# Performance work log

Measured on AMD Instinct MI355X. Metric: run time of the kernel, lower is better.

The kernel has to match this reference:

```python
import jax, jax.numpy as jnp
import numpy as np

EMBED_DIM = 2048
HIDDEN_DIM = 2048
SEQ_LEN = 8192


def setup_inputs() -> dict:
    key = jax.random.key(0)
    ks = jax.random.split(key, 6)
    x = jax.random.normal(ks[0], (SEQ_LEN, EMBED_DIM), dtype=jnp.float32)
    # original uses torch.rand (uniform [0,1)) for params
    W_h = jax.random.uniform(ks[1], (HIDDEN_DIM, HIDDEN_DIM), dtype=jnp.float32)
    W_x = jax.random.uniform(ks[2], (HIDDEN_DIM, EMBED_DIM), dtype=jnp.float32)
    W_y = jax.random.uniform(ks[3], (EMBED_DIM, HIDDEN_DIM), dtype=jnp.float32)
    B_h = jax.random.uniform(ks[4], (HIDDEN_DIM,), dtype=jnp.float32)
    B_y = jax.random.uniform(ks[5], (EMBED_DIM,), dtype=jnp.float32)
    return {"x": x, "W_h": W_h, "W_x": W_x, "W_y": W_y, "B_h": B_h, "B_y": B_y}


def reference(x, W_h, W_x, W_y, B_h, B_y):
    # Precompute input projections for all timesteps in one GEMM: [T, H]
    xp = x @ W_x.T + B_h

    def step(h, xp_t):
        h_new = jnp.tanh(W_h @ h + xp_t)  # [H]
        return h_new, h_new

    h0 = jnp.zeros((W_h.shape[0],), dtype=x.dtype)
    h_final, hs = jax.lax.scan(step, h0, xp)  # hs: [T, H]
    # Output projection + softmax over embed dim, batched over timesteps
    logits = hs @ W_y.T + B_y  # [T, E]
    output = jax.nn.softmax(logits, axis=-1)
    return (h_final, output)
```

## Files before the change

kernel.cpp:

```cpp
#include <hip/hip_runtime.h>

#define T_SEQ 8192
#define HDIM  2048
#define EDIM  2048
#define RBLK  64
#define ROWS_PER_BLK (HDIM / RBLK)

typedef unsigned long long u64;
typedef __attribute__((ext_vector_type(4))) unsigned int u32x4;
typedef __attribute__((ext_vector_type(4))) float f32x4;

__device__ inline void poll_pair(const u64* p0, const u64* p1, u32x4& a, u32x4& b) {
    asm volatile("global_load_dwordx4 %0, %2, off sc1\n\t"
                 "global_load_dwordx4 %1, %3, off sc1\n\t"
                 "s_waitcnt vmcnt(0)"
                 : "=v"(a), "=v"(b) : "v"(p0), "v"(p1) : "memory");
}

__device__ inline f32x4 ld_w16(const float* p) {
    f32x4 r;
    asm volatile("global_load_dwordx4 %0, %1, off" : "=v"(r) : "v"(p));
    return r;
}

__device__ inline float fast_tanh(float z) {
    float zc = fminf(fmaxf(z, -15.f), 15.f);
    float zs = zc * 2.88539008177792681f;
    float ez; asm("v_exp_f32 %0, %1" : "=v"(ez) : "v"(zs));
    float rc; float ezp = ez + 1.f;
    asm("v_rcp_f32 %0, %1" : "=v"(rc) : "v"(ezp));
    return (ez - 1.f) * rc;
}

__global__ __launch_bounds__(256) void gemm_nt_bias(
    const float* __restrict__ A, const float* __restrict__ B,
    const float* __restrict__ bias, float* __restrict__ C,
    int M, int N, int K)
{
    constexpr int BK = 32;
    __shared__ float As[BK][64 + 4];
    __shared__ float Bs[BK][64 + 4];

    const int tx = threadIdx.x & 15;
    const int ty = threadIdx.x >> 4;
    const int m0 = blockIdx.y * 64;
    const int n0 = blockIdx.x * 64;

    float acc[4][4] = {};

    for (int kk = 0; kk < K; kk += BK) {
        #pragma unroll
        for (int p = 0; p < 8; ++p) {
            int idx = p * 256 + threadIdx.x;
            int r = idx >> 5;
            int c = idx & 31;
            As[c][r] = A[(size_t)(m0 + r) * K + kk + c];
            Bs[c][r] = B[(size_t)(n0 + r) * K + kk + c];
        }
        __syncthreads();
        #pragma unroll
        for (int k = 0; k < BK; ++k) {
            float4 a = *(const float4*)&As[k][ty * 4];
            float4 b = *(const float4*)&Bs[k][tx * 4];
            float av[4] = {a.x, a.y, a.z, a.w};
            float bv[4] = {b.x, b.y, b.z, b.w};
            #pragma unroll
            for (int i = 0; i < 4; ++i)
                #pragma unroll
                for (int j = 0; j < 4; ++j)
                    acc[i][j] = fmaf(av[i], bv[j], acc[i][j]);
        }
        __syncthreads();
    }

    float4 bb = *(const float4*)&bias[n0 + tx * 4];
    float bvv[4] = {bb.x, bb.y, bb.z, bb.w};
    #pragma unroll
    for (int i = 0; i < 4; ++i) {
        float4 o;
        o.x = acc[i][0] + bvv[0];
        o.y = acc[i][1] + bvv[1];
        o.z = acc[i][2] + bvv[2];
        o.w = acc[i][3] + bvv[3];
        *(float4*)&C[(size_t)(m0 + ty * 4 + i) * N + n0 + tx * 4] = o;
    }
}

__global__ __launch_bounds__(256) void gemm_nt_bias_tc(
    const float* __restrict__ A, const float* __restrict__ B,
    const float* __restrict__ bias, float* __restrict__ Ct,
    int M, int N, int K)
{
    constexpr int BK = 32;
    __shared__ float As[BK][64 + 4];
    __shared__ float Bs[BK][64 + 4];

    const int tx = threadIdx.x & 15;
    const int ty = threadIdx.x >> 4;
    const int m0 = blockIdx.y * 64;
    const int n0 = blockIdx.x * 64;

    float acc[4][4] = {};

    for (int kk = 0; kk < K; kk += BK) {
        #pragma unroll
        for (int p = 0; p < 8; ++p) {
            int idx = p * 256 + threadIdx.x;
            int r = idx >> 5;
            int c = idx & 31;
            As[c][r] = A[(size_t)(m0 + r) * K + kk + c];
            Bs[c][r] = B[(size_t)(n0 + r) * K + kk + c];
        }
        __syncthreads();
        #pragma unroll
        for (int k = 0; k < BK; ++k) {
            float4 a = *(const float4*)&As[k][ty * 4];
            float4 b = *(const float4*)&Bs[k][tx * 4];
            float av[4] = {a.x, a.y, a.z, a.w};
            float bv[4] = {b.x, b.y, b.z, b.w};
            #pragma unroll
            for (int i = 0; i < 4; ++i)
                #pragma unroll
                for (int j = 0; j < 4; ++j)
                    acc[i][j] = fmaf(av[i], bv[j], acc[i][j]);
        }
        __syncthreads();
    }

    float4 bb = *(const float4*)&bias[n0 + tx * 4];
    float bvv[4] = {bb.x, bb.y, bb.z, bb.w};
    #pragma unroll
    for (int j = 0; j < 4; ++j) {
        float4 o;
        o.x = acc[0][j] + bvv[j];
        o.y = acc[1][j] + bvv[j];
        o.z = acc[2][j] + bvv[j];
        o.w = acc[3][j] + bvv[j];
        *(float4*)&Ct[(size_t)(n0 + tx * 4 + j) * M + m0 + ty * 4] = o;
    }
}

__global__ __launch_bounds__(512, 1) void rnn_recurrence(
    const float* __restrict__ Wh, const float* __restrict__ xpT,
    float* __restrict__ Hs, u64* __restrict__ hbuf, int T)
{
    const int tid  = threadIdx.x;
    const int lane = tid & 63;
    const int wid  = tid >> 6;
    const int r0   = blockIdx.x * ROWS_PER_BLK + wid * 4;

    const float* wr0 = Wh + (size_t)(r0 + 0) * HDIM + lane * 4;
    const float* wr1 = Wh + (size_t)(r0 + 1) * HDIM + lane * 4;
    const float* wr2 = Wh + (size_t)(r0 + 2) * HDIM + lane * 4;
    const float* wr3 = Wh + (size_t)(r0 + 3) * HDIM + lane * 4;

    f32x4 w00 = ld_w16(wr0 + 0*256), w01 = ld_w16(wr0 + 1*256), w02 = ld_w16(wr0 + 2*256), w03 = ld_w16(wr0 + 3*256);
    f32x4 w04 = ld_w16(wr0 + 4*256), w05 = ld_w16(wr0 + 5*256), w06 = ld_w16(wr0 + 6*256), w07 = ld_w16(wr0 + 7*256);
    f32x4 w10 = ld_w16(wr1 + 0*256), w11 = ld_w16(wr1 + 1*256), w12 = ld_w16(wr1 + 2*256), w13 = ld_w16(wr1 + 3*256);
    f32x4 w14 = ld_w16(wr1 + 4*256), w15 = ld_w16(wr1 + 5*256), w16 = ld_w16(wr1 + 6*256), w17 = ld_w16(wr1 + 7*256);
    f32x4 w20 = ld_w16(wr2 + 0*256), w21 = ld_w16(wr2 + 1*256), w22 = ld_w16(wr2 + 2*256), w23 = ld_w16(wr2 + 3*256);
    f32x4 w24 = ld_w16(wr2 + 4*256), w25 = ld_w16(wr2 + 5*256), w26 = ld_w16(wr2 + 6*256), w27 = ld_w16(wr2 + 7*256);
    f32x4 w30 = ld_w16(wr3 + 0*256), w31 = ld_w16(wr3 + 1*256), w32 = ld_w16(wr3 + 2*256), w33 = ld_w16(wr3 + 3*256);
    f32x4 w34 = ld_w16(wr3 + 4*256), w35 = ld_w16(wr3 + 5*256), w36 = ld_w16(wr3 + 6*256), w37 = ld_w16(wr3 + 7*256);
    asm volatile("s_waitcnt vmcnt(0)" ::: "memory");

    __shared__ float hsm[HDIM];

    for (int t = 0; t < T; ++t) {
        float xq = 0.f;
        if (lane < 4) xq = xpT[(size_t)(r0 + lane) * T + t];

        float sv = 0.f;
        if (t > 0) {
            const u64* hb = hbuf + (size_t)(t & 1) * HDIM;
            const unsigned tg = (unsigned)t;
            const u64* p0 = hb + 2 * tid;
            const u64* p1 = hb + 1024 + 2 * tid;

            u32x4 a, b;
            poll_pair(p0, p1, a, b);
            while ((a.y != tg) | (a.w != tg) | (b.y != tg) | (b.w != tg))
                poll_pair(p0, p1, a, b);

            ((float2*)hsm)[tid] =
                make_float2(__uint_as_float(a.x), __uint_as_float(a.z));
            ((float2*)hsm)[tid + 512] =
                make_float2(__uint_as_float(b.x), __uint_as_float(b.z));
            __syncthreads();

            float s0 = 0.f, s1 = 0.f, s2 = 0.f, s3 = 0.f;
            #define RNN_STEP(IDX, WA, WB, WC, WD)                                   \
            {   float4 h4 = ((const float4*)hsm)[(IDX) * 64 + lane];                \
                s0 = fmaf(WA.x, h4.x, s0); s0 = fmaf(WA.y, h4.y, s0);               \
                s0 = fmaf(WA.z, h4.z, s0); s0 = fmaf(WA.w, h4.w, s0);               \
                s1 = fmaf(WB.x, h4.x, s1); s1 = fmaf(WB.y, h4.y, s1);               \
                s1 = fmaf(WB.z, h4.z, s1); s1 = fmaf(WB.w, h4.w, s1);               \
                s2 = fmaf(WC.x, h4.x, s2); s2 = fmaf(WC.y, h4.y, s2);               \
                s2 = fmaf(WC.z, h4.z, s2); s2 = fmaf(WC.w, h4.w, s2);               \
                s3 = fmaf(WD.x, h4.x, s3); s3 = fmaf(WD.y, h4.y, s3);               \
                s3 = fmaf(WD.z, h4.z, s3); s3 = fmaf(WD.w, h4.w, s3); }
            RNN_STEP(0, w00, w10, w20, w30)
            RNN_STEP(1, w01, w11, w21, w31)
            RNN_STEP(2, w02, w12, w22, w32)
            RNN_STEP(3, w03, w13, w23, w33)
            RNN_STEP(4, w04, w14, w24, w34)
            RNN_STEP(5, w05, w15, w25, w35)
            RNN_STEP(6, w06, w16, w26, w36)
            RNN_STEP(7, w07, w17, w27, w37)
            #undef RNN_STEP

            float fa = (lane & 1) ? s1 : s0;
            float fb = (lane & 1) ? s0 : s1;
            fa += __shfl_xor(fb, 1);
            float fc = (lane & 1) ? s3 : s2;
            float fd = (lane & 1) ? s2 : s3;
            fc += __shfl_xor(fd, 1);
            float fe = (lane & 2) ? fc : fa;
            float ff = (lane & 2) ? fa : fc;
            fe += __shfl_xor(ff, 2);
            #pragma unroll
            for (int off = 4; off < 64; off <<= 1) fe += __shfl_xor(fe, off);
            sv = fe;
        }

        if (lane < 4) {
            float hn = fast_tanh(sv + xq);
            u64 pk = ((u64)(unsigned)(t + 1) << 32) | (u64)__float_as_uint(hn);
            (void)__hip_atomic_exchange(
                &hbuf[(size_t)((t + 1) & 1) * HDIM + r0 + lane], pk,
                __ATOMIC_RELAXED, __HIP_MEMORY_SCOPE_AGENT);
            Hs[(size_t)t * HDIM + r0 + lane] = hn;
        }
    }
}

__global__ __launch_bounds__(256) void softmax_rows(
    const float* __restrict__ logits, float* __restrict__ out)
{
    const int row = blockIdx.x;
    const float4* in4 = (const float4*)(logits + (size_t)row * EDIM);
    float4* out4 = (float4*)(out + (size_t)row * EDIM);

    float4 v0 = in4[threadIdx.x];
    float4 v1 = in4[threadIdx.x + 256];

    float m = fmaxf(fmaxf(fmaxf(v0.x, v0.y), fmaxf(v0.z, v0.w)),
                    fmaxf(fmaxf(v1.x, v1.y), fmaxf(v1.z, v1.w)));
    #pragma unroll
    for (int off = 32; off > 0; off >>= 1) m = fmaxf(m, __shfl_xor(m, off));

    __shared__ float red[4];
    if ((threadIdx.x & 63) == 0) red[threadIdx.x >> 6] = m;
    __syncthreads();
    m = fmaxf(fmaxf(red[0], red[1]), fmaxf(red[2], red[3]));
    __syncthreads();

    float e[8];
    e[0] = expf(v0.x - m); e[1] = expf(v0.y - m);
    e[2] = expf(v0.z - m); e[3] = expf(v0.w - m);
    e[4] = expf(v1.x - m); e[5] = expf(v1.y - m);
    e[6] = expf(v1.z - m); e[7] = expf(v1.w - m);

    float s = e[0] + e[1] + e[2] + e[3] + e[4] + e[5] + e[6] + e[7];
    #pragma unroll
    for (int off = 32; off > 0; off >>= 1) s += __shfl_xor(s, off);
    if ((threadIdx.x & 63) == 0) red[threadIdx.x >> 6] = s;
    __syncthreads();
    s = red[0] + red[1] + red[2] + red[3];

    float inv = 1.0f / s;
    out4[threadIdx.x]       = make_float4(e[0] * inv, e[1] * inv, e[2] * inv, e[3] * inv);
    out4[threadIdx.x + 256] = make_float4(e[4] * inv, e[5] * inv, e[6] * inv, e[7] * inv);
}

__global__ void copy_vec(const float* __restrict__ src, float* __restrict__ dst, int n)
{
    int i = blockIdx.x * blockDim.x + threadIdx.x;
    if (i < n) dst[i] = src[i];
}

extern "C" void kernel_launch(void* const* d_in, const int* in_sizes, int n_in,
                              void* d_out, int out_size, void* d_ws, size_t ws_size,
                              hipStream_t stream)
{
    const float* x  = (const float*)d_in[0];
    const float* Wh = (const float*)d_in[1];
    const float* Wx = (const float*)d_in[2];
    const float* Wy = (const float*)d_in[3];
    const float* Bh = (const float*)d_in[4];
    const float* By = (const float*)d_in[5];

    float* out    = (float*)d_out;
    float* hfinal = out;
    float* hs     = out + HDIM;

    float* xpT  = (float*)d_ws;
    u64*   hbuf = (u64*)((char*)d_ws + (size_t)T_SEQ * HDIM * 4);
    float* logits = xpT;

    hipMemsetAsync(hbuf, 0, 2 * HDIM * sizeof(u64), stream);

    gemm_nt_bias_tc<<<dim3(HDIM / 64, T_SEQ / 64), 256, 0, stream>>>(
        x, Wx, Bh, xpT, T_SEQ, HDIM, EDIM);

    int T = T_SEQ;
    const float* xpT_c = xpT;
    void* args[] = {(void*)&Wh, (void*)&xpT_c, (void*)&hs, (void*)&hbuf, (void*)&T};
    hipLaunchCooperativeKernel((void*)rnn_recurrence, dim3(RBLK), dim3(512),
                               args, 0, stream);

    gemm_nt_bias<<<dim3(EDIM / 64, T_SEQ / 64), 256, 0, stream>>>(
        hs, Wy, By, logits, T_SEQ, EDIM, HDIM);

    copy_vec<<<dim3(HDIM / 256), 256, 0, stream>>>(
        hs + (size_t)(T_SEQ - 1) * HDIM, hfinal, HDIM);

    softmax_rows<<<dim3(T_SEQ), 256, 0, stream>>>(logits, hs);
}
```

Before: 14.82 ms.

## Repartition recurrence so each thread owns a column slice of all block rows

The recurrent matvec is restructured so each thread holds 4 columns for all 32 rows of its block, instead of each wave owning 4 rows across all columns. Each thread now polls only the 4 hidden values it needs from global memory, which drops the shared-memory broadcast of the full hidden state. Partial sums are combined with a multi-row butterfly shuffle, then a shared-memory cross-wave sum performed by a single wave. This trades the full-vector LDS staging for more shuffle work and an extra barrier per step, and concentrates the tanh and publish on one wave.

```diff
diff --git a/kernel.cpp b/kernel.cpp
--- a/kernel.cpp
+++ b/kernel.cpp
@@ -4,7 +4,6 @@
 #define HDIM  2048
 #define EDIM  2048
 #define RBLK  64
-#define ROWS_PER_BLK (HDIM / RBLK)
 
 typedef unsigned long long u64;
 typedef __attribute__((ext_vector_type(4))) unsigned int u32x4;
@@ -147,89 +146,72 @@
     const int tid  = threadIdx.x;
     const int lane = tid & 63;
     const int wid  = tid >> 6;
-    const int r0   = blockIdx.x * ROWS_PER_BLK + wid * 4;
-
-    const float* wr0 = Wh + (size_t)(r0 + 0) * HDIM + lane * 4;
-    const float* wr1 = Wh + (size_t)(r0 + 1) * HDIM + lane * 4;
-    const float* wr2 = Wh + (size_t)(r0 + 2) * HDIM + lane * 4;
-    const float* wr3 = Wh + (size_t)(r0 + 3) * HDIM + lane * 4;
-
-    f32x4 w00 = ld_w16(wr0 + 0*256), w01 = ld_w16(wr0 + 1*256), w02 = ld_w16(wr0 + 2*256), w03 = ld_w16(wr0 + 3*256);
-    f32x4 w04 = ld_w16(wr0 + 4*256), w05 = ld_w16(wr0 + 5*256), w06 = ld_w16(wr0 + 6*256), w07 = ld_w16(wr0 + 7*256);
-    f32x4 w10 = ld_w16(wr1 + 0*256), w11 = ld_w16(wr1 + 1*256), w12 = ld_w16(wr1 + 2*256), w13 = ld_w16(wr1 + 3*256);
-    f32x4 w14 = ld_w16(wr1 + 4*256), w15 = ld_w16(wr1 + 5*256), w16 = ld_w16(wr1 + 6*256), w17 = ld_w16(wr1 + 7*256);
-    f32x4 w20 = ld_w16(wr2 + 0*256), w21 = ld_w16(wr2 + 1*256), w22 = ld_w16(wr2 + 2*256), w23 = ld_w16(wr2 + 3*256);
-    f32x4 w24 = ld_w16(wr2 + 4*256), w25 = ld_w16(wr2 + 5*256), w26 = ld_w16(wr2 + 6*256), w27 = ld_w16(wr2 + 7*256);
-    f32x4 w30 = ld_w16(wr3 + 0*256), w31 = ld_w16(wr3 + 1*256), w32 = ld_w16(wr3 + 2*256), w33 = ld_w16(wr3 + 3*256);
-    f32x4 w34 = ld_w16(wr3 + 4*256), w35 = ld_w16(wr3 + 5*256), w36 = ld_w16(wr3 + 6*256), w37 = ld_w16(wr3 + 7*256);
+    const int r0   = blockIdx.x * 32;
+    const int c0   = tid * 4;
+
+    f32x4 w[32];
+    #pragma unroll
+    for (int r = 0; r < 32; ++r)
+        w[r] = ld_w16(Wh + (size_t)(r0 + r) * HDIM + c0);
     asm volatile("s_waitcnt vmcnt(0)" ::: "memory");
 
-    __shared__ float hsm[HDIM];
+    __shared__ float pw[8 * 32];
 
     for (int t = 0; t < T; ++t) {
-        float xq = 0.f;
-        if (lane < 4) xq = xpT[(size_t)(r0 + lane) * T + t];
-
-        float sv = 0.f;
         if (t > 0) {
-            const u64* hb = hbuf + (size_t)(t & 1) * HDIM;
+            const u64* hb = hbuf + (size_t)(t & 1) * HDIM + c0;
             const unsigned tg = (unsigned)t;
-            const u64* p0 = hb + 2 * tid;
-            const u64* p1 = hb + 1024 + 2 * tid;
 
             u32x4 a, b;
-            poll_pair(p0, p1, a, b);
+            poll_pair(hb, hb + 2, a, b);
             while ((a.y != tg) | (a.w != tg) | (b.y != tg) | (b.w != tg))
-                poll_pair(p0, p1, a, b);
-
-            ((float2*)hsm)[tid] =
-                make_float2(__uint_as_float(a.x), __uint_as_float(a.z));
-            ((float2*)hsm)[tid + 512] =
-                make_float2(__uint_as_float(b.x), __uint_as_float(b.z));
-            __syncthreads();
-
-            float s0 = 0.f, s1 = 0.f, s2 = 0.f, s3 = 0.f;
-            #define RNN_STEP(IDX, WA, WB, WC, WD)                                   \
-            {   float4 h4 = ((const float4*)hsm)[(IDX) * 64 + lane];                \
-                s0 = fmaf(WA.x, h4.x, s0); s0 = fmaf(WA.y, h4.y, s0);               \
-                s0 = fmaf(WA.z, h4.z, s0); s0 = fmaf(WA.w, h4.w, s0);               \
-                s1 = fmaf(WB.x, h4.x, s1); s1 = fmaf(WB.y, h4.y, s1);               \
-                s1 = fmaf(WB.z, h4.z, s1); s1 = fmaf(WB.w, h4.w, s1);               \
-                s2 = fmaf(WC.x, h4.x, s2); s2 = fmaf(WC.y, h4.y, s2);               \
-                s2 = fmaf(WC.z, h4.z, s2); s2 = fmaf(WC.w, h4.w, s2);               \
-                s3 = fmaf(WD.x, h4.x, s3); s3 = fmaf(WD.y, h4.y, s3);               \
-                s3 = fmaf(WD.z, h4.z, s3); s3 = fmaf(WD.w, h4.w, s3); }
-            RNN_STEP(0, w00, w10, w20, w30)
-            RNN_STEP(1, w01, w11, w21, w31)
-            RNN_STEP(2, w02, w12, w22, w32)
-            RNN_STEP(3, w03, w13, w23, w33)
-            RNN_STEP(4, w04, w14, w24, w34)
-            RNN_STEP(5, w05, w15, w25, w35)
-            RNN_STEP(6, w06, w16, w26, w36)
-            RNN_STEP(7, w07, w17, w27, w37)
-            #undef RNN_STEP
-
-            float fa = (lane & 1) ? s1 : s0;
-            float fb = (lane & 1) ? s0 : s1;
-            fa += __shfl_xor(fb, 1);
-            float fc = (lane & 1) ? s3 : s2;
-            float fd = (lane & 1) ? s2 : s3;
-            fc += __shfl_xor(fd, 1);
-            float fe = (lane & 2) ? fc : fa;
-            float ff = (lane & 2) ? fa : fc;
-            fe += __shfl_xor(ff, 2);
+                poll_pair(hb, hb + 2, a, b);
+
+            const float h0 = __uint_as_float(a.x), h1 = __uint_as_float(a.z);
+            const float h2 = __uint_as_float(b.x), h3 = __uint_as_float(b.z);
+
+            float s[32];
             #pragma unroll
-            for (int off = 4; off < 64; off <<= 1) fe += __shfl_xor(fe, off);
-            sv = fe;
-        }
-
-        if (lane < 4) {
-            float hn = fast_tanh(sv + xq);
-            u64 pk = ((u64)(unsigned)(t + 1) << 32) | (u64)__float_as_uint(hn);
-            (void)__hip_atomic_exchange(
-                &hbuf[(size_t)((t + 1) & 1) * HDIM + r0 + lane], pk,
-                __ATOMIC_RELAXED, __HIP_MEMORY_SCOPE_AGENT);
-            Hs[(size_t)t * HDIM + r0 + lane] = hn;
+            for (int r = 0; r < 32; ++r) {
+                float acc =      w[r].x * h0;
+                acc = fmaf(w[r].y, h1, acc);
+                acc = fmaf(w[r].z, h2, acc);
+                acc = fmaf(w[r].w, h3, acc);
+                s[r] = acc;
+            }
+
+            #pragma unroll
+            for (int step = 0; step < 5; ++step) {
+                const int off = 1 << step;
+                const bool up = (lane & off) != 0;
+                #pragma unroll
+                for (int j = 0; j < (32 >> (step + 1)); ++j) {
+                    float aa = s[2 * j], bb = s[2 * j + 1];
+                    float lo = up ? bb : aa;
+                    float hi = up ? aa : bb;
+                    s[j] = lo + __shfl_xor(hi, off);
+                }
+            }
+            float rowsum = s[0] + __shfl_xor(s[0], 32);
+            if (lane < 32) pw[wid * 32 + lane] = rowsum;
+        }
+        __syncthreads();
+
+        if (wid == 0) {
+            const int l = lane & 31;
+            float sum = 0.f;
+            if (t > 0) {
+                #pragma unroll
+                for (int k = 0; k < 8; ++k) sum += pw[k * 32 + l];
+            }
+            float xq = xpT[(size_t)(r0 + l) * T + t];
+            float hn = fast_tanh(sum + xq);
+            if (lane < 32) {
+                u64 pk = ((u64)(unsigned)(t + 1) << 32) | (u64)__float_as_uint(hn);
+                __hip_atomic_store(&hbuf[(size_t)((t + 1) & 1) * HDIM + r0 + lane],
+                                   pk, __ATOMIC_RELAXED, __HIP_MEMORY_SCOPE_AGENT);
+                Hs[(size_t)t * HDIM + r0 + lane] = hn;
+            }
         }
     }
 }
```

Measured after the change: 21.73 ms. +46.6%, slower.
